# Performance work log

Hardware: AMD Instinct MI355X
Metric: run time of the kernel (lower is better)

## Reference

```python
import jax, jax.numpy as jnp
import numpy as np

B, T = 32, 32
I, H, O = 8192, 8192, 2048
NNZ_HH, NNZ_IH, NNZ_HO = 1_048_576, 524_288, 262_144


def spmm(rows, cols, vals, n_out, x):
    # COO sparse (n_out, n_in) @ x (n_in, B) -> (n_out, B).
    # Duplicate (row,col) pairs sum, matching torch_sparse.coalesce semantics.
    return jax.ops.segment_sum(vals[:, None] * x[cols], rows, num_segments=n_out)


def setup_inputs() -> dict:
    key = jax.random.key(0)
    ks = jax.random.split(key, 10)
    x = jax.random.normal(ks[0], (B, T, I), jnp.float32)
    hh_rows = jax.random.randint(ks[1], (NNZ_HH,), 0, H)
    hh_cols = jax.random.randint(ks[2], (NNZ_HH,), 0, H)
    hh_vals = jax.random.normal(ks[3], (NNZ_HH,), jnp.float32) * 0.02
    hh_bias = jnp.zeros((H, 1), jnp.float32)
    ih_rows = jax.random.randint(ks[4], (NNZ_IH,), 0, H)
    ih_cols = jax.random.randint(ks[5], (NNZ_IH,), 0, I)
    ih_vals = jax.random.normal(ks[6], (NNZ_IH,), jnp.float32) * 0.02
    ho_rows = jax.random.randint(ks[7], (NNZ_HO,), 0, O)
    ho_cols = jax.random.randint(ks[8], (NNZ_HO,), 0, H)
    ho_vals = jax.random.normal(ks[9], (NNZ_HO,), jnp.float32) * 0.02
    ho_bias = jnp.zeros((O, 1), jnp.float32)
    return dict(x=x, hh_rows=hh_rows, hh_cols=hh_cols, hh_vals=hh_vals,
                hh_bias=hh_bias, ih_rows=ih_rows, ih_cols=ih_cols,
                ih_vals=ih_vals, ho_rows=ho_rows, ho_cols=ho_cols,
                ho_vals=ho_vals, ho_bias=ho_bias)


def reference(x, hh_rows, hh_cols, hh_vals, hh_bias,
              ih_rows, ih_cols, ih_vals,
              ho_rows, ho_cols, ho_vals, ho_bias):
    # batch_first (B, T, I) -> time-major feature-first (T, I, B)
    xs = jnp.transpose(x, (1, 2, 0))
    h0 = jnp.zeros((H, B), x.dtype)  # default_hidden_init_fn='zeros'

    def step(h, x_t):
        pre = (spmm(ih_rows, ih_cols, ih_vals, H, x_t)  # ih (bias_ih=False)
               + spmm(hh_rows, hh_cols, hh_vals, H, h)
               + hh_bias)
        h_new = jax.nn.sigmoid(pre)  # nonlinearity='Sigmoid'
        out_t = spmm(ho_rows, ho_cols, ho_vals, O, h_new) + ho_bias
        return h_new, out_t

    _, outs = jax.lax.scan(step, h0, xs)  # outs: (T, O, B)
    return jnp.transpose(outs, (2, 0, 1))  # (B, T, O)
```

## Files before the change

kernel.cpp:

```cpp
#include <hip/hip_runtime.h>
#include <hip/hip_fp16.h>

constexpr int Bb = 32;
constexpr int Tt = 32;
constexpr int Ii = 8192;
constexpr int Hh = 8192;
constexpr int Oo = 2048;
constexpr int TB = Tt * Bb;
constexpr int TILE = 2048;
constexpr int FBR = 32;
constexpr int NFB_H = Hh / FBR;
constexpr int NFB_O = Oo / FBR;


__device__ __forceinline__ float entval(uint32_t u) {
  return __half2float(__ushort_as_half((unsigned short)(u >> 16)));
}

__global__ void transpose_x_kernel(const float* __restrict__ x, __half2* __restrict__ x2) {
  int blk = blockIdx.x;
  int tp = blk >> 7;
  int ib = blk & 127;
  int t0 = tp * 2;
  int i0 = ib * 64;
  __shared__ float lds[64][65];
  int tid = threadIdx.x;
  for (int idx = tid; idx < 64 * 64; idx += 256) {
    int row = idx >> 6, il = idx & 63;
    int tt = row >> 5, bb = row & 31;
    lds[il][row] = x[(size_t)bb * Tt * Ii + (size_t)(t0 + tt) * Ii + i0 + il];
  }
  __syncthreads();
  for (int idx = tid; idx < 64 * 32; idx += 256) {
    int il = idx >> 5;
    int q = idx & 31;
    int tt = q >> 4, p = q & 15;
    float lo = lds[il][tt * 32 + 2 * p];
    float hi = lds[il][tt * 32 + 2 * p + 1];
    x2[(size_t)(i0 + il) * (TB / 2) + (size_t)(t0 + tt) * 16 + p] = __floats2half2_rn(lo, hi);
  }
}

__global__ void __launch_bounds__(256) count_kernel(
    const int* __restrict__ r1, int n1, int* __restrict__ tb1, int nt1,
    const int* __restrict__ r2, int n2, int* __restrict__ tb2, int nt2,
    const int* __restrict__ r3, int n3, int* __restrict__ tb3) {
  __shared__ int cnt[NFB_H];
  int tile = blockIdx.x;
  const int* rows; int n; int* tb; int tl; int nfb;
  if (tile < nt1)            { rows = r1; n = n1; tb = tb1; tl = tile;             nfb = NFB_H; }
  else if (tile < nt1 + nt2) { rows = r2; n = n2; tb = tb2; tl = tile - nt1;       nfb = NFB_H; }
  else                       { rows = r3; n = n3; tb = tb3; tl = tile - nt1 - nt2; nfb = NFB_O; }
  for (int i = threadIdx.x; i < nfb; i += 256) cnt[i] = 0;
  __syncthreads();
  int base = tl * TILE;
  for (int k = threadIdx.x; k < TILE; k += 256) {
    int j = base + k;
    if (j < n) atomicAdd(&cnt[rows[j] >> 5], 1);
  }
  __syncthreads();
  for (int i = threadIdx.x; i < nfb; i += 256) tb[tl * nfb + i] = cnt[i];
}

__global__ void __launch_bounds__(256) scan_col_kernel(
    int* __restrict__ tb1, int nt1, int* __restrict__ tb2, int nt2,
    int* __restrict__ tb3, int nt3, int* __restrict__ totals) {
  __shared__ int sums[256];
  int col = blockIdx.x;
  int* tb; int nt; int fb; int nfb;
  if (col < NFB_H)          { tb = tb1; nt = nt1; fb = col;             nfb = NFB_H; }
  else if (col < 2 * NFB_H) { tb = tb2; nt = nt2; fb = col - NFB_H;     nfb = NFB_H; }
  else                      { tb = tb3; nt = nt3; fb = col - 2 * NFB_H; nfb = NFB_O; }
  int tid = threadIdx.x;
  int nper = (nt + 255) >> 8;
  int vals[8];
  int t0 = tid * nper;
  int a = 0;
  for (int i = 0; i < nper; i++) {
    int t = t0 + i;
    vals[i] = (t < nt) ? tb[t * nfb + fb] : 0;
    a += vals[i];
  }
  sums[tid] = a;
  __syncthreads();
  for (int off = 1; off < 256; off <<= 1) {
    int o = (tid >= off) ? sums[tid - off] : 0;
    __syncthreads();
    sums[tid] += o;
    __syncthreads();
  }
  int run = sums[tid] - a;
  for (int i = 0; i < nper; i++) {
    int t = t0 + i;
    if (t < nt) { tb[t * nfb + fb] = run; run += vals[i]; }
  }
  if (tid == 255) totals[col] = sums[255];
}

__global__ void __launch_bounds__(256) scan_base_kernel(
    const int* __restrict__ totals, int* __restrict__ fbb1,
    int* __restrict__ fbb2, int* __restrict__ fbb3) {
  __shared__ int s[256];
  int m = blockIdx.x;
  const int* t; int* fbb; int nfb;
  if (m == 0)      { t = totals;             fbb = fbb1; nfb = NFB_H; }
  else if (m == 1) { t = totals + NFB_H;     fbb = fbb2; nfb = NFB_H; }
  else             { t = totals + 2 * NFB_H; fbb = fbb3; nfb = NFB_O; }
  int tid = threadIdx.x;
  int v = (tid < nfb) ? t[tid] : 0;
  s[tid] = v;
  __syncthreads();
  for (int off = 1; off < 256; off <<= 1) {
    int o = (tid >= off) ? s[tid - off] : 0;
    __syncthreads();
    s[tid] += o;
    __syncthreads();
  }
  if (tid < nfb) fbb[tid] = s[tid] - v;
  if (tid == 255) fbb[nfb] = s[255];
}

__global__ void __launch_bounds__(256) place_kernel(
    const int* __restrict__ r1, const int* __restrict__ c1, const float* __restrict__ v1,
    int n1, const int* __restrict__ tb1, int nt1, const int* __restrict__ fbb1, uint64_t* __restrict__ s1,
    const int* __restrict__ r2, const int* __restrict__ c2, const float* __restrict__ v2,
    int n2, const int* __restrict__ tb2, int nt2, const int* __restrict__ fbb2, uint64_t* __restrict__ s2,
    const int* __restrict__ r3, const int* __restrict__ c3, const float* __restrict__ v3,
    int n3, const int* __restrict__ tb3, const int* __restrict__ fbb3, uint64_t* __restrict__ s3) {
  __shared__ int cnt[NFB_H];
  __shared__ int incl[NFB_H];
  __shared__ uint64_t stg[TILE];
  __shared__ int gad[TILE];
  int tile = blockIdx.x;
  const int* rows; const int* cols; const float* vals; int n;
  const int* tb; const int* fbb; uint64_t* st; int tl; int nfb;
  if (tile < nt1)            { rows = r1; cols = c1; vals = v1; n = n1; tb = tb1; fbb = fbb1; st = s1; tl = tile;             nfb = NFB_H; }
  else if (tile < nt1 + nt2) { rows = r2; cols = c2; vals = v2; n = n2; tb = tb2; fbb = fbb2; st = s2; tl = tile - nt1;       nfb = NFB_H; }
  else                       { rows = r3; cols = c3; vals = v3; n = n3; tb = tb3; fbb = fbb3; st = s3; tl = tile - nt1 - nt2; nfb = NFB_O; }
  int tid = threadIdx.x;
  for (int i = tid; i < NFB_H; i += 256) cnt[i] = 0;
  __syncthreads();
  constexpr int E = TILE / 256;
  uint32_t entv[E]; int rowv[E]; int rnkv[E];
  int base = tl * TILE;
  for (int k = 0; k < E; k++) {
    int j = base + k * 256 + tid;
    if (j < n) {
      int rr = rows[j];
      rowv[k] = rr;
      entv[k] = ((uint32_t)__half_as_ushort(__float2half_rn(vals[j])) << 16) | (uint32_t)cols[j];
      rnkv[k] = atomicAdd(&cnt[rr >> 5], 1);
    } else {
      rowv[k] = -1;
    }
  }
  __syncthreads();
  int v0 = cnt[tid];
  incl[tid] = v0;
  __syncthreads();
  for (int off = 1; off < 256; off <<= 1) {
    int o = (tid >= off) ? incl[tid - off] : 0;
    __syncthreads();
    incl[tid] += o;
    __syncthreads();
  }
  int total = incl[255];
  for (int k = 0; k < E; k++) {
    if (rowv[k] >= 0) {
      int fb = rowv[k] >> 5;
      int slot = (incl[fb] - cnt[fb]) + rnkv[k];
      stg[slot] = ((uint64_t)entv[k] << 32) | (uint32_t)rowv[k];
      gad[slot] = fbb[fb] + tb[tl * nfb + fb] + rnkv[k];
    }
  }
  __syncthreads();
  for (int i = tid; i < total; i += 256) st[gad[i]] = stg[i];
}

__global__ void __launch_bounds__(256) rowcount_kernel(
    const uint64_t* __restrict__ s1, const int* __restrict__ fbb1, int* __restrict__ cu1,
    const uint64_t* __restrict__ s2, const int* __restrict__ fbb2, int* __restrict__ cu2,
    const uint64_t* __restrict__ s3, const int* __restrict__ fbb3, int* __restrict__ cu3) {
  __shared__ int rc[FBR];
  int bx = blockIdx.x;
  const uint64_t* st; const int* fbb; int* cu; int b;
  if (bx < NFB_H)          { st = s1; fbb = fbb1; cu = cu1; b = bx; }
  else if (bx < 2 * NFB_H) { st = s2; fbb = fbb2; cu = cu2; b = bx - NFB_H; }
  else                     { st = s3; fbb = fbb3; cu = cu3; b = bx - 2 * NFB_H; }
  int tid = threadIdx.x;
  if (tid < FBR) rc[tid] = 0;
  __syncthreads();
  int lo = fbb[b], hi = fbb[b + 1];
  for (int j = lo + tid; j < hi; j += 256)
    atomicAdd(&rc[(int)(uint32_t)st[j] & (FBR - 1)], 1);
  __syncthreads();
  if (tid < FBR) cu[(b << 5) + tid] = rc[tid];
}

__global__ void scan_csr_kernel(int* __restrict__ c1, int n1, int* __restrict__ r1,
                                int* __restrict__ c2, int n2, int* __restrict__ r2,
                                int* __restrict__ c3, int n3, int* __restrict__ r3) {
  __shared__ int sums[1024];
  int bx = blockIdx.x;
  int tid = threadIdx.x;
  int* cnt_cursor; int n; int* row_start;
  if (bx == 0)      { cnt_cursor = c1; n = n1; row_start = r1; }
  else if (bx == 1) { cnt_cursor = c2; n = n2; row_start = r2; }
  else              { cnt_cursor = c3; n = n3; row_start = r3; }
  int chunk = (n + 1023) >> 10;
  int base = tid * chunk;
  int s = 0;
  for (int i = 0; i < chunk; i++) {
    int idx = base + i;
    if (idx < n) s += (cnt_cursor[idx] + 15) & ~15;
  }
  sums[tid] = s;
  __syncthreads();
  for (int off = 1; off < 1024; off <<= 1) {
    int other = (tid >= off) ? sums[tid - off] : 0;
    __syncthreads();
    sums[tid] += other;
    __syncthreads();
  }
  int run = sums[tid] - s;
  for (int i = 0; i < chunk; i++) {
    int idx = base + i;
    if (idx < n) {
      int v = cnt_cursor[idx];
      row_start[idx] = run;
      cnt_cursor[idx] = run + v;
      run += (v + 15) & ~15;
    }
  }
  if (tid == 1023) row_start[n] = sums[1023];
}

__global__ void __launch_bounds__(256) csort_kernel(
    const uint64_t* __restrict__ s1, const int* __restrict__ fbb1, const int* __restrict__ rs1, uint32_t* __restrict__ e1,
    const uint64_t* __restrict__ s2, const int* __restrict__ fbb2, const int* __restrict__ rs2, uint32_t* __restrict__ e2,
    const uint64_t* __restrict__ s3, const int* __restrict__ fbb3, const int* __restrict__ rs3, uint32_t* __restrict__ e3) {
  __shared__ uint32_t ob[8192];
  __shared__ int rcnt[FBR];
  __shared__ int rsl[FBR + 1];
  int bx = blockIdx.x;
  const uint64_t* st; const int* fbb; const int* rs; uint32_t* e; int b;
  if (bx < NFB_H)            { st = s1; fbb = fbb1; rs = rs1; e = e1; b = bx; }
  else if (bx < 2 * NFB_H)   { st = s2; fbb = fbb2; rs = rs2; e = e2; b = bx - NFB_H; }
  else                       { st = s3; fbb = fbb3; rs = rs3; e = e3; b = bx - 2 * NFB_H; }
  int tid = threadIdx.x;
  if (tid <= FBR) rsl[tid] = rs[(b << 5) + tid];
  if (tid < FBR) rcnt[tid] = 0;
  __syncthreads();
  int reg0 = rsl[0];
  int rlen = rsl[FBR] - reg0;
  int lo = fbb[b], hi = fbb[b + 1];
  if (rlen <= 8192) {
    for (int i = tid; i < rlen; i += 256) ob[i] = 0;
    __syncthreads();
    for (int j = lo + tid; j < hi; j += 256) {
      uint64_t v = st[j];
      int rl = (int)(uint32_t)v & (FBR - 1);
      int rk = atomicAdd(&rcnt[rl], 1);
      ob[(rsl[rl] - reg0) + rk] = (uint32_t)(v >> 32);
    }
    __syncthreads();
    for (int i = tid; i < rlen; i += 256) e[reg0 + i] = ob[i];
  } else {
    for (int i = tid; i < rlen; i += 256) e[reg0 + i] = 0;
    __syncthreads();
    for (int j = lo + tid; j < hi; j += 256) {
      uint64_t v = st[j];
      int rl = (int)(uint32_t)v & (FBR - 1);
      int rk = atomicAdd(&rcnt[rl], 1);
      e[rsl[rl] + rk] = (uint32_t)(v >> 32);
    }
  }
}

__global__ void __launch_bounds__(256, 4) preih_kernel(
    const int* __restrict__ ih_rs, const int* __restrict__ ih_cur,
    const uint32_t* __restrict__ ih_ent,
    const float* __restrict__ hh_bias, const __half* __restrict__ x2h,
    __half2* __restrict__ preAll) {
  int r = blockIdx.x * 4 + (threadIdx.x >> 6);
  int lane = threadIdx.x & 63;
  int s0  = __builtin_amdgcn_readfirstlane(ih_rs[r]);
  int cnt = __builtin_amdgcn_readfirstlane(ih_cur[r]) - s0;
  int nb = (cnt + 7) >> 3;
  const int4* ep = (const int4*)(ih_ent + s0);
  const uint32_t* xb = (const uint32_t*)x2h;

  float2 a[8];
  #pragma unroll
  for (int k = 0; k < 8; k++) a[k] = {0.f, 0.f};
  int4 f0 = ep[0], f1 = ep[1];
  for (int i = 0; i < nb; i++) {
    int4 e0 = f0, e1 = f1;
    f0 = ep[2 * i + 2];
    f1 = ep[2 * i + 3];
    uint32_t uu[8] = {(uint32_t)e0.x, (uint32_t)e0.y, (uint32_t)e0.z, (uint32_t)e0.w,
                      (uint32_t)e1.x, (uint32_t)e1.y, (uint32_t)e1.z, (uint32_t)e1.w};
    #pragma unroll
    for (int j = 0; j < 8; j++) {
      uint32_t u = uu[j];
      const uint32_t* cb = xb + (size_t)(u & 0xffff) * (TB / 2) + lane;
      float v = entval(u);
      #pragma unroll
      for (int k = 0; k < 8; k++) {
        uint32_t g = cb[k * 64];
        float2 xv = __half22float2(*(__half2*)&g);
        a[k].x += v * xv.x;
        a[k].y += v * xv.y;
      }
    }
  }
  float bias = hh_bias[r];
  int tq = lane >> 4, p = lane & 15;
  #pragma unroll
  for (int k = 0; k < 8; k++) {
    int t = k * 4 + tq;
    preAll[((size_t)t * Hh + r) * 16 + p] = __floats2half2_rn(a[k].x + bias, a[k].y + bias);
  }
}

__global__ void __launch_bounds__(256, 8) step_kernel(
    const int* __restrict__ hh_rs, const int* __restrict__ hh_cur,
    const uint32_t* __restrict__ hh_ent,
    const __half* __restrict__ pre_t,
    const __half* __restrict__ hprev,
    __half* __restrict__ hnext) {
  int r = (blockIdx.x * 256 + threadIdx.x) >> 6;
  int lane = threadIdx.x & 63;
  int q = lane >> 4, p = lane & 15;
  int s0  = __builtin_amdgcn_readfirstlane(hh_rs[r]);
  int cnt = __builtin_amdgcn_readfirstlane(hh_cur[r]) - s0;
  int nb = (cnt + 15) >> 4;
  const int4* ep = (const int4*)(hh_ent + s0);
  const uint32_t* hp = (const uint32_t*)hprev;
  uint32_t pu = ((const uint32_t*)pre_t)[(r << 4) + p];
  float2 pre2 = __half22float2(*(__half2*)&pu);

  float2 a0 = {0.f, 0.f}, a1 = {0.f, 0.f};
  int4 f = ep[q];
  for (int i = 0; i < nb; i++) {
    int4 e = f;
    f = ep[4 * (i + 1) + q];
    uint32_t u0 = (uint32_t)e.x, u1 = (uint32_t)e.y, u2 = (uint32_t)e.z, u3 = (uint32_t)e.w;
    uint32_t g0 = hp[((u0 & 0xffff) << 4) + p];
    uint32_t g1 = hp[((u1 & 0xffff) << 4) + p];
    uint32_t g2 = hp[((u2 & 0xffff) << 4) + p];
    uint32_t g3 = hp[((u3 & 0xffff) << 4) + p];
    float v0 = entval(u0), v1 = entval(u1), v2 = entval(u2), v3 = entval(u3);
    float2 x0 = __half22float2(*(__half2*)&g0), x1 = __half22float2(*(__half2*)&g1);
    float2 x2v = __half22float2(*(__half2*)&g2), x3 = __half22float2(*(__half2*)&g3);
    a0.x += v0 * x0.x;  a0.y += v0 * x0.y;
    a1.x += v1 * x1.x;  a1.y += v1 * x1.y;
    a0.x += v2 * x2v.x; a0.y += v2 * x2v.y;
    a1.x += v3 * x3.x;  a1.y += v3 * x3.y;
  }
  float ax = a0.x + a1.x, ay = a0.y + a1.y;
  ax += __shfl_xor(ax, 16, 64);  ay += __shfl_xor(ay, 16, 64);
  ax += __shfl_xor(ax, 32, 64);  ay += __shfl_xor(ay, 32, 64);
  float hv0 = 1.0f / (1.0f + __expf(-(pre2.x + ax)));
  float hv1 = 1.0f / (1.0f + __expf(-(pre2.y + ay)));
  if (q == 0) ((__half2*)hnext)[(r << 4) + p] = __floats2half2_rn(hv0, hv1);
}

__global__ void __launch_bounds__(256, 8) out_kernel(
    const int* __restrict__ ho_rs, const int* __restrict__ ho_cur,
    const uint32_t* __restrict__ ho_ent,
    const float* __restrict__ ho_bias, const __half* __restrict__ hAll,
    float* __restrict__ out_tmp) {
  int xcd = blockIdx.x & 7;
  int w   = (blockIdx.x >> 3) * 4 + (threadIdx.x >> 6);
  int lane = threadIdx.x & 63;
  int h = lane >> 5, b = lane & 31;
  int t0 = xcd * 4;
  constexpr size_t HS = (size_t)Hh * Bb;
  const __half* hbase = hAll + (size_t)(t0 + 1) * HS;

  for (int o = w; o < Oo; o += 1024) {
    int s0  = __builtin_amdgcn_readfirstlane(ho_rs[o]);
    int cnt = __builtin_amdgcn_readfirstlane(ho_cur[o]) - s0;
    int nb = (cnt + 7) >> 3;
    const int4* ep = (const int4*)(ho_ent + s0);
    float bias = (h == 0) ? ho_bias[o] : 0.f;
    float A0 = bias, A1 = bias, A2 = bias, A3 = bias;
    float B0 = 0.f, B1 = 0.f, B2 = 0.f, B3 = 0.f;
    for (int i = 0; i < nb; i++) {
      int4 e0 = ep[2 * i], e1 = ep[2 * i + 1];
      uint32_t u0 = (uint32_t)(h ? e0.y : e0.x);
      uint32_t u1 = (uint32_t)(h ? e0.w : e0.z);
      uint32_t u2 = (uint32_t)(h ? e1.y : e1.x);
      uint32_t u3 = (uint32_t)(h ? e1.w : e1.z);
      const __half* p0 = hbase + (((size_t)(u0 & 0xffff)) << 5) + b;
      const __half* p1 = hbase + (((size_t)(u1 & 0xffff)) << 5) + b;
      const __half* p2 = hbase + (((size_t)(u2 & 0xffff)) << 5) + b;
      const __half* p3 = hbase + (((size_t)(u3 & 0xffff)) << 5) + b;
      float v0 = entval(u0), v1 = entval(u1), v2 = entval(u2), v3 = entval(u3);
      A0 += v0 * __half2float(p0[0]);
      A1 += v0 * __half2float(p0[HS]);
      A2 += v0 * __half2float(p0[2 * HS]);
      A3 += v0 * __half2float(p0[3 * HS]);
      B0 += v1 * __half2float(p1[0]);
      B1 += v1 * __half2float(p1[HS]);
      B2 += v1 * __half2float(p1[2 * HS]);
      B3 += v1 * __half2float(p1[3 * HS]);
      A0 += v2 * __half2float(p2[0]);
      A1 += v2 * __half2float(p2[HS]);
      A2 += v2 * __half2float(p2[2 * HS]);
      A3 += v2 * __half2float(p2[3 * HS]);
      B0 += v3 * __half2float(p3[0]);
      B1 += v3 * __half2float(p3[HS]);
      B2 += v3 * __half2float(p3[2 * HS]);
      B3 += v3 * __half2float(p3[3 * HS]);
    }
    A0 += B0; A1 += B1; A2 += B2; A3 += B3;
    A0 += __shfl_xor(A0, 32, 64);
    A1 += __shfl_xor(A1, 32, 64);
    A2 += __shfl_xor(A2, 32, 64);
    A3 += __shfl_xor(A3, 32, 64);
    if (h == 0) {
      out_tmp[((size_t)(t0 + 0) * Oo + o) * Bb + b] = A0;
      out_tmp[((size_t)(t0 + 1) * Oo + o) * Bb + b] = A1;
      out_tmp[((size_t)(t0 + 2) * Oo + o) * Bb + b] = A2;
      out_tmp[((size_t)(t0 + 3) * Oo + o) * Bb + b] = A3;
    }
  }
}

__global__ void transpose_out_kernel(const float* __restrict__ out_tmp, float* __restrict__ dout) {
  int blk = blockIdx.x;
  int t  = blk >> 5;
  int o0 = (blk & 31) << 6;
  __shared__ float lds[64][33];
  int tid = threadIdx.x;
  for (int idx = tid; idx < 64 * 32; idx += 256) {
    int ol = idx >> 5, bb = idx & 31;
    lds[ol][bb] = out_tmp[(size_t)t * Oo * Bb + (size_t)(o0 + ol) * Bb + bb];
  }
  __syncthreads();
  for (int idx = tid; idx < 32 * 64; idx += 256) {
    int bb = idx >> 6, ol = idx & 63;
    dout[(size_t)bb * Tt * Oo + (size_t)t * Oo + o0 + ol] = lds[ol][bb];
  }
}

extern "C" void kernel_launch(void* const* d_in, const int* in_sizes, int n_in,
                              void* d_out, int out_size, void* d_ws, size_t ws_size,
                              hipStream_t stream) {
  const float* x       = (const float*)d_in[0];
  const int*   hh_rows = (const int*)d_in[1];
  const int*   hh_cols = (const int*)d_in[2];
  const float* hh_vals = (const float*)d_in[3];
  const float* hh_bias = (const float*)d_in[4];
  const int*   ih_rows = (const int*)d_in[5];
  const int*   ih_cols = (const int*)d_in[6];
  const float* ih_vals = (const float*)d_in[7];
  const int*   ho_rows = (const int*)d_in[8];
  const int*   ho_cols = (const int*)d_in[9];
  const float* ho_vals = (const float*)d_in[10];
  const float* ho_bias = (const float*)d_in[11];
  float* out = (float*)d_out;

  const int nnz_hh = in_sizes[1];
  const int nnz_ih = in_sizes[5];
  const int nnz_ho = in_sizes[8];

  const int ntile_ih = (nnz_ih + TILE - 1) / TILE;
  const int ntile_hh = (nnz_hh + TILE - 1) / TILE;
  const int ntile_ho = (nnz_ho + TILE - 1) / TILE;

  char* w = (char*)d_ws;
  size_t off = 0;
  auto alloc = [&](size_t bytes) -> void* {
    void* p = w + off;
    off += (bytes + 255) & ~(size_t)255;
    return p;
  };
  __half* x2h    = (__half*)alloc(2 * (size_t)Ii * TB);
  __half* hAll   = (__half*)alloc(2 * (size_t)(Tt + 1) * Hh * Bb);
  __half* preAll = (__half*)alloc(2 * (size_t)Tt * Hh * Bb);
  float* out_tmp = (float*)alloc(4 * (size_t)Tt * Oo * Bb);
  int*  ih_rs  = (int*)alloc(4 * (size_t)(Hh + 1));
  int*  hh_rs  = (int*)alloc(4 * (size_t)(Hh + 1));
  int*  ho_rs  = (int*)alloc(4 * (size_t)(Oo + 1));
  int*  cur_all = (int*)alloc(4 * (size_t)(Hh + Hh + Oo));
  int*  ih_cur = cur_all;
  int*  hh_cur = cur_all + Hh;
  int*  ho_cur = cur_all + 2 * Hh;
  uint32_t* ih_ent = (uint32_t*)alloc(4 * ((size_t)nnz_ih + 16 * Hh + 64));
  uint32_t* hh_ent = (uint32_t*)alloc(4 * ((size_t)nnz_hh + 16 * Hh + 64));
  uint32_t* ho_ent = (uint32_t*)alloc(4 * ((size_t)nnz_ho + 16 * Oo + 64));
  int* tb_ih  = (int*)alloc(4 * (size_t)(ntile_ih * NFB_H));
  int* tb_hh  = (int*)alloc(4 * (size_t)(ntile_hh * NFB_H));
  int* tb_ho  = (int*)alloc(4 * (size_t)(ntile_ho * NFB_O));
  int* fbb_ih = (int*)alloc(4 * (size_t)(NFB_H + 1));
  int* fbb_hh = (int*)alloc(4 * (size_t)(NFB_H + 1));
  int* fbb_ho = (int*)alloc(4 * (size_t)(NFB_O + 1));
  int* totals = (int*)alloc(4 * (size_t)(2 * NFB_H + NFB_O));

  uint64_t* s_ih = (uint64_t*)preAll;
  uint64_t* s_hh = s_ih + (size_t)nnz_ih;
  uint64_t* s_ho = s_hh + (size_t)nnz_hh;

  hipMemsetAsync(hAll, 0, 2 * (size_t)Hh * Bb, stream);

  transpose_x_kernel<<<(Tt / 2) * (Ii / 64), 256, 0, stream>>>(x, (__half2*)x2h);

  count_kernel<<<ntile_ih + ntile_hh + ntile_ho, 256, 0, stream>>>(
      ih_rows, nnz_ih, tb_ih, ntile_ih,
      hh_rows, nnz_hh, tb_hh, ntile_hh,
      ho_rows, nnz_ho, tb_ho);
  scan_col_kernel<<<2 * NFB_H + NFB_O, 256, 0, stream>>>(
      tb_ih, ntile_ih, tb_hh, ntile_hh, tb_ho, ntile_ho, totals);
  scan_base_kernel<<<3, 256, 0, stream>>>(totals, fbb_ih, fbb_hh, fbb_ho);
  place_kernel<<<ntile_ih + ntile_hh + ntile_ho, 256, 0, stream>>>(
      ih_rows, ih_cols, ih_vals, nnz_ih, tb_ih, ntile_ih, fbb_ih, s_ih,
      hh_rows, hh_cols, hh_vals, nnz_hh, tb_hh, ntile_hh, fbb_hh, s_hh,
      ho_rows, ho_cols, ho_vals, nnz_ho, tb_ho, fbb_ho, s_ho);
  rowcount_kernel<<<2 * NFB_H + NFB_O, 256, 0, stream>>>(
      s_ih, fbb_ih, ih_cur, s_hh, fbb_hh, hh_cur, s_ho, fbb_ho, ho_cur);
  scan_csr_kernel<<<3, 1024, 0, stream>>>(
      ih_cur, Hh, ih_rs, hh_cur, Hh, hh_rs, ho_cur, Oo, ho_rs);
  csort_kernel<<<2 * NFB_H + NFB_O, 256, 0, stream>>>(
      s_ih, fbb_ih, ih_rs, ih_ent,
      s_hh, fbb_hh, hh_rs, hh_ent,
      s_ho, fbb_ho, ho_rs, ho_ent);

  preih_kernel<<<Hh / 4, 256, 0, stream>>>(
      ih_rs, ih_cur, ih_ent, hh_bias, x2h, (__half2*)preAll);

  for (int t = 0; t < Tt; t++) {
    step_kernel<<<Hh / 4, 256, 0, stream>>>(
        hh_rs, hh_cur, hh_ent,
        preAll + (size_t)t * Hh * Bb,
        hAll + (size_t)t * Hh * Bb,
        hAll + (size_t)(t + 1) * Hh * Bb);
  }

  out_kernel<<<2048, 256, 0, stream>>>(
      ho_rs, ho_cur, ho_ent, ho_bias, hAll, out_tmp);
  transpose_out_kernel<<<Tt * (Oo / 64), 256, 0, stream>>>(out_tmp, out);

  (void)n_in; (void)out_size; (void)ws_size;
}
```

Before: 604.6 us.

## Split preih kernel across time chunks per XCD to raise parallelism

```diff
diff --git a/kernel.cpp b/kernel.cpp
--- a/kernel.cpp
+++ b/kernel.cpp
@@ -7,6 +7,7 @@
 constexpr int Hh = 8192;
 constexpr int Oo = 2048;
 constexpr int TB = Tt * Bb;
+constexpr int TCH = 4;
 constexpr int TILE = 2048;
 constexpr int FBR = 32;
 constexpr int NFB_H = Hh / FBR;
@@ -277,50 +278,53 @@
   }
 }
 
-__global__ void __launch_bounds__(256, 4) preih_kernel(
+__global__ void __launch_bounds__(256, 8) preih_kernel(
     const int* __restrict__ ih_rs, const int* __restrict__ ih_cur,
     const uint32_t* __restrict__ ih_ent,
     const float* __restrict__ hh_bias, const __half* __restrict__ x2h,
     __half2* __restrict__ preAll) {
-  int r = blockIdx.x * 4 + (threadIdx.x >> 6);
+  int xcd = blockIdx.x & 7;
+  int r = ((blockIdx.x >> 3) << 2) + (threadIdx.x >> 6);
   int lane = threadIdx.x & 63;
+  int t0 = xcd * TCH;
   int s0  = __builtin_amdgcn_readfirstlane(ih_rs[r]);
   int cnt = __builtin_amdgcn_readfirstlane(ih_cur[r]) - s0;
   int nb = (cnt + 7) >> 3;
   const int4* ep = (const int4*)(ih_ent + s0);
-  const uint32_t* xb = (const uint32_t*)x2h;
-
-  float2 a[8];
-  #pragma unroll
-  for (int k = 0; k < 8; k++) a[k] = {0.f, 0.f};
+  const uint32_t* xb = (const uint32_t*)(x2h + (size_t)t0 * Bb);
+
+  float2 a0 = {0.f, 0.f}, a1 = {0.f, 0.f}, a2 = {0.f, 0.f}, a3 = {0.f, 0.f};
   int4 f0 = ep[0], f1 = ep[1];
   for (int i = 0; i < nb; i++) {
     int4 e0 = f0, e1 = f1;
     f0 = ep[2 * i + 2];
     f1 = ep[2 * i + 3];
-    uint32_t uu[8] = {(uint32_t)e0.x, (uint32_t)e0.y, (uint32_t)e0.z, (uint32_t)e0.w,
-                      (uint32_t)e1.x, (uint32_t)e1.y, (uint32_t)e1.z, (uint32_t)e1.w};
-    #pragma unroll
-    for (int j = 0; j < 8; j++) {
-      uint32_t u = uu[j];
-      const uint32_t* cb = xb + (size_t)(u & 0xffff) * (TB / 2) + lane;
-      float v = entval(u);
-      #pragma unroll
-      for (int k = 0; k < 8; k++) {
-        uint32_t g = cb[k * 64];
-        float2 xv = __half22float2(*(__half2*)&g);
-        a[k].x += v * xv.x;
-        a[k].y += v * xv.y;
-      }
-    }
+    uint32_t u0 = (uint32_t)e0.x, u1 = (uint32_t)e0.y, u2 = (uint32_t)e0.z, u3 = (uint32_t)e0.w;
+    uint32_t u4 = (uint32_t)e1.x, u5 = (uint32_t)e1.y, u6 = (uint32_t)e1.z, u7 = (uint32_t)e1.w;
+    uint32_t g0 = xb[(size_t)(u0 & 0xffff) * (TB / 2) + lane];
+    uint32_t g1 = xb[(size_t)(u1 & 0xffff) * (TB / 2) + lane];
+    uint32_t g2 = xb[(size_t)(u2 & 0xffff) * (TB / 2) + lane];
+    uint32_t g3 = xb[(size_t)(u3 & 0xffff) * (TB / 2) + lane];
+    uint32_t g4 = xb[(size_t)(u4 & 0xffff) * (TB / 2) + lane];
+    uint32_t g5 = xb[(size_t)(u5 & 0xffff) * (TB / 2) + lane];
+    uint32_t g6 = xb[(size_t)(u6 & 0xffff) * (TB / 2) + lane];
+    uint32_t g7 = xb[(size_t)(u7 & 0xffff) * (TB / 2) + lane];
+    float v0 = entval(u0), v1 = entval(u1), v2 = entval(u2), v3 = entval(u3);
+    float v4 = entval(u4), v5 = entval(u5), v6 = entval(u6), v7 = entval(u7);
+    float2 x0 = __half22float2(*(__half2*)&g0), x1 = __half22float2(*(__half2*)&g1);
+    float2 x2v = __half22float2(*(__half2*)&g2), x3 = __half22float2(*(__half2*)&g3);
+    float2 x4 = __half22float2(*(__half2*)&g4), x5 = __half22float2(*(__half2*)&g5);
+    float2 x6 = __half22float2(*(__half2*)&g6), x7 = __half22float2(*(__half2*)&g7);
+    a0.x += v0 * x0.x;  a0.y += v0 * x0.y;   a0.x += v4 * x4.x;  a0.y += v4 * x4.y;
+    a1.x += v1 * x1.x;  a1.y += v1 * x1.y;   a1.x += v5 * x5.x;  a1.y += v5 * x5.y;
+    a2.x += v2 * x2v.x; a2.y += v2 * x2v.y;  a2.x += v6 * x6.x;  a2.y += v6 * x6.y;
+    a3.x += v3 * x3.x;  a3.y += v3 * x3.y;   a3.x += v7 * x7.x;  a3.y += v7 * x7.y;
   }
   float bias = hh_bias[r];
-  int tq = lane >> 4, p = lane & 15;
-  #pragma unroll
-  for (int k = 0; k < 8; k++) {
-    int t = k * 4 + tq;
-    preAll[((size_t)t * Hh + r) * 16 + p] = __floats2half2_rn(a[k].x + bias, a[k].y + bias);
-  }
+  float sx = ((a0.x + a1.x) + (a2.x + a3.x)) + bias;
+  float sy = ((a0.y + a1.y) + (a2.y + a3.y)) + bias;
+  int tt = lane >> 4, p = lane & 15;
+  preAll[((size_t)(t0 + tt) * Hh + r) * 16 + p] = __floats2half2_rn(sx, sy);
 }
 
 __global__ void __launch_bounds__(256, 8) step_kernel(
@@ -528,7 +532,7 @@
       s_hh, fbb_hh, hh_rs, hh_ent,
       s_ho, fbb_ho, ho_rs, ho_ent);
 
-  preih_kernel<<<Hh / 4, 256, 0, stream>>>(
+  preih_kernel<<<8 * Hh / 4, 256, 0, stream>>>(
       ih_rs, ih_cur, ih_ent, hh_bias, x2h, (__half2*)preAll);
 
   for (int t = 0; t < Tt; t++) {
```

Measured after the change: 534.2 us. 1.13x faster.
